# Kernel tuning notes

Hardware: AMD Instinct MI355X
Metric: run time of the kernel (lower is better)

## Reference

```python
import jax, jax.numpy as jnp
import numpy as np
from jax import lax

B, S, DM = 2, 2048, 2048
H, HKV, D = 16, 4, 128          # heads, kv heads, head_dim = DM // H
CLAMP_MAX = 0.95


def setup_inputs() -> dict:
    key = jax.random.key(0)
    k0, k1, k2, k3 = jax.random.split(key, 4)
    w_scale = 2 ** (-2.5) * (6.0 / (DM + DM)) ** 0.5  # xavier_uniform gain 2^-2.5 scale
    return {
        "hidden_states": jax.random.normal(k0, (B, S, DM), dtype=jnp.float32),
        "Wq": jax.random.uniform(k1, (DM, DM), jnp.float32, -w_scale, w_scale),
        "bq": jnp.zeros((DM,), jnp.float32),
        "Wk": jax.random.uniform(k2, (HKV * D, DM), jnp.float32, -w_scale, w_scale),
        "bk": jnp.zeros((HKV * D,), jnp.float32),
        "Wv": jax.random.uniform(k3, (HKV * D, DM), jnp.float32, -w_scale, w_scale),
        "bv": jnp.zeros((HKV * D,), jnp.float32),
    }


def _gla_forward(hidden_states, Wq, bq, Wk, bk, Wv, bv):
    b, s, _ = hidden_states.shape
    q = hidden_states @ Wq.T + bq                      # [b, s, H*D]
    k = hidden_states @ Wk.T + bk                      # [b, s, HKV*D]
    v = hidden_states @ Wv.T + bv                      # [b, s, HKV*D]
    q = q.reshape(b, s, H, D).transpose(0, 2, 1, 3)    # [b, H, s, D]
    k = k.reshape(b, s, HKV, D).transpose(0, 2, 1, 3)  # [b, HKV, s, D]
    v = v.reshape(b, s, HKV, D).transpose(0, 2, 1, 3)
    rep = H // HKV                                     # repeat_kv (GQA)
    k = jnp.repeat(k, rep, axis=1)                     # [b, H, s, D]
    v = jnp.repeat(v, rep, axis=1)
    q = jax.nn.relu(q)                                 # q_feature_map
    # layer_idx == 0 gate path: k = clamp(sigmoid(k), max=0.95); g = log(1 - k)
    kf = jnp.minimum(jax.nn.sigmoid(k.astype(jnp.float32)), CLAMP_MAX)
    g = jnp.log1p(-kf)                                 # log-space decay, g <= log(0.05) < 0 ... 0
    k = kf.astype(v.dtype)
    scale = D ** -0.5                                  # fla gla default scale = head_dim**-0.5
    q = (q * scale).astype(v.dtype)

    # GLA recurrence over time: S_t = exp(g_t)[:,None] * S_{t-1} + k_t^T v_t ; o_t = q_t S_t
    qs = q.transpose(2, 0, 1, 3)   # [s, b, H, D]
    ks = k.transpose(2, 0, 1, 3)
    vs = v.transpose(2, 0, 1, 3)
    gs = g.transpose(2, 0, 1, 3)

    def step(state, inp):           # state: [b, H, D, D] (key_dim x value_dim)
        qt, kt, vt, gt = inp
        state = state * jnp.exp(gt)[..., :, None] + kt[..., :, None] * vt[..., None, :]
        ot = jnp.einsum('bhd,bhde->bhe', qt, state)
        return state, ot

    S0 = jnp.zeros((b, H, D, D), jnp.float32)
    _, o = lax.scan(step, S0, (qs, ks, vs, gs))        # o: [s, b, H, D]
    o = o.transpose(1, 0, 2, 3).reshape(b, s, H * D)   # 'b h l d -> b l (h d)'
    return o


def reference(hidden_states, Wq, bq, Wk, bk, Wv, bv):
    return _gla_forward(hidden_states, Wq, bq, Wk, bk, Wv, bv)
```

## Files before the change

kernel.cpp:

```cpp
#include <hip/hip_runtime.h>
#include <math.h>

#define B_ 2
#define S_ 2048
#define DM_ 2048
#define H_ 16
#define HKV_ 4
#define D_ 128
#define NKV_ 512
#define M_ 4096
#define CHK_ 32
#define NC_ 64
#define SCALE_ 0.08838834764831845f
#define CLAMP_ 0.95f

typedef unsigned short u16;
typedef u16 ushortx8 __attribute__((ext_vector_type(8)));
typedef __bf16 bf16x8 __attribute__((ext_vector_type(8)));
typedef float f32x4 __attribute__((ext_vector_type(4)));

#define ASYNC16(gsrc, ldst) \
  __builtin_amdgcn_global_load_lds((const __attribute__((address_space(1))) void*)(gsrc), \
                                   (__attribute__((address_space(3))) void*)(ldst), 16, 0, 0)

__device__ __forceinline__ u16 f2b(float x){
  unsigned u = __float_as_uint(x);
  return (u16)((u + 0x7FFFu + ((u >> 16) & 1u)) >> 16);
}
__device__ __forceinline__ float b2f(u16 h){
  return __uint_as_float(((unsigned)h) << 16);
}
__device__ __forceinline__ bf16x8 ld8(const u16* p){
  return __builtin_bit_cast(bf16x8, *(const ushortx8*)p);
}
__device__ __forceinline__ f32x4 mfma16(bf16x8 a, bf16x8 b, f32x4 c){
  return __builtin_amdgcn_mfma_f32_16x16x32_bf16(a, b, c, 0, 0, 0);
}

__global__ void k_cvt_all(const float* __restrict__ hs, const float* __restrict__ Wq,
                          const float* __restrict__ Wk, const float* __restrict__ Wv,
                          u16* __restrict__ hsb, u16* __restrict__ wcb){
  int i = blockIdx.x * blockDim.x + threadIdx.x;
  const float* src; u16* dst;
  if (i < 1048576)      { src = hs + (size_t)i * 8;               dst = hsb + (size_t)i * 8; }
  else if (i < 1572864) { int j = i - 1048576; src = Wq + (size_t)j * 8; dst = wcb + (size_t)j * 8; }
  else if (i < 1703936) { int j = i - 1572864; src = Wk + (size_t)j * 8; dst = wcb + 4194304 + (size_t)j * 8; }
  else                  { int j = i - 1703936; src = Wv + (size_t)j * 8; dst = wcb + 5242880 + (size_t)j * 8; }
  const float4* p = (const float4*)src;
  float4 a = p[0], c = p[1];
  ushortx8 o;
  o[0]=f2b(a.x); o[1]=f2b(a.y); o[2]=f2b(a.z); o[3]=f2b(a.w);
  o[4]=f2b(c.x); o[5]=f2b(c.y); o[6]=f2b(c.z); o[7]=f2b(c.w);
  *(ushortx8*)dst = o;
}

__launch_bounds__(256, 2)
__global__ void k_gemm(const u16* __restrict__ A, const u16* __restrict__ W,
                       const float* __restrict__ bq, const float* __restrict__ bk,
                       const float* __restrict__ bv,
                       u16* __restrict__ qp, u16* __restrict__ kp,
                       float* __restrict__ gG, u16* __restrict__ vT){
  __shared__ u16 Al[128 * 32];
  __shared__ u16 Bl[128 * 32];
  const int tid = threadIdx.x;
  const int wid = tid >> 6, lane = tid & 63;
  const int m0 = blockIdx.y * 128, n0 = blockIdx.x * 128;
  const int wr = (wid >> 1) * 64, wc = (wid & 1) * 64;
  const int lr = lane & 15, lk = (lane >> 4) * 8;
  f32x4 acc[4][4] = {};
  for (int kt = 0; kt < 64; ++kt){
    const int k0 = kt * 32;
    #pragma unroll
    for (int s = 0; s < 2; ++s){
      const int fo = (wid * 2 + s) * 512;
      const int el = fo + lane * 8;
      const int row = el >> 5, kk = el & 31;
      ASYNC16(A + (size_t)(m0 + row) * DM_ + k0 + kk, Al + fo);
      ASYNC16(W + (size_t)(n0 + row) * DM_ + k0 + kk, Bl + fo);
    }
    __syncthreads();
    bf16x8 af[4], bfr[4];
    #pragma unroll
    for (int i = 0; i < 4; ++i) af[i]  = ld8(&Al[(wr + i*16 + lr)*32 + lk]);
    #pragma unroll
    for (int j = 0; j < 4; ++j) bfr[j] = ld8(&Bl[(wc + j*16 + lr)*32 + lk]);
    #pragma unroll
    for (int i = 0; i < 4; ++i)
      #pragma unroll
      for (int j = 0; j < 4; ++j)
        acc[i][j] = mfma16(af[i], bfr[j], acc[i][j]);
    __syncthreads();
  }
  const int lg4 = lane >> 4;
  const int tn = blockIdx.x;
  if (tn < 16){
    #pragma unroll
    for (int i = 0; i < 4; ++i){
      const int rb = m0 + wr + i*16 + lg4*4;
      #pragma unroll
      for (int j = 0; j < 4; ++j){
        const int col = n0 + wc + j*16 + lr;
        const float bb = bq[col];
        #pragma unroll
        for (int r = 0; r < 4; ++r){
          float q = fmaxf(acc[i][j][r] + bb, 0.f) * SCALE_;
          qp[(size_t)(rb + r) * DM_ + col] = f2b(q);
        }
      }
    }
  } else if (tn < 20){
    #pragma unroll
    for (int i = 0; i < 4; ++i){
      const int rb = m0 + wr + i*16 + lg4*4;
      #pragma unroll
      for (int j = 0; j < 4; ++j){
        const int cc = n0 - DM_ + wc + j*16 + lr;
        const float bb = bk[cc];
        #pragma unroll
        for (int r = 0; r < 4; ++r){
          float x = acc[i][j][r] + bb;
          float kf = fminf(1.f / (1.f + __expf(-x)), CLAMP_);
          kp[(size_t)(rb + r) * NKV_ + cc] = f2b(kf);
          gG[(size_t)(rb + r) * NKV_ + cc] = log1pf(-kf);
        }
      }
    }
  } else {
    #pragma unroll
    for (int i = 0; i < 4; ++i){
      const int rb = m0 + wr + i*16 + lg4*4;
      const int bb_ = rb >> 11;
      const int srow = rb & 2047;
      #pragma unroll
      for (int j = 0; j < 4; ++j){
        const int cc = n0 - DM_ - NKV_ + wc + j*16 + lr;
        const float bias = bv[cc];
        const int kv = cc >> 7, e = cc & 127;
        ushort4 pk;
        pk.x = f2b(acc[i][j][0] + bias);
        pk.y = f2b(acc[i][j][1] + bias);
        pk.z = f2b(acc[i][j][2] + bias);
        pk.w = f2b(acc[i][j][3] + bias);
        *(ushort4*)(vT + (((size_t)(bb_ * HKV_ + kv) * D_ + e) * S_ + srow)) = pk;
      }
    }
  }
}

__global__ void k_cumsum(float* __restrict__ g, float* __restrict__ dec){
  const int c = blockIdx.x, b = blockIdx.y;
  const int col = threadIdx.x;
  const size_t base = ((size_t)b * S_ + (size_t)c * CHK_) * NKV_ + col;
  float v[CHK_];
  #pragma unroll
  for (int t = 0; t < CHK_; ++t) v[t] = g[base + (size_t)t * NKV_];
  float acc = 0.f;
  #pragma unroll
  for (int t = 0; t < CHK_; ++t){ acc += v[t]; v[t] = acc; }
  #pragma unroll
  for (int t = 0; t < CHK_; ++t) g[base + (size_t)t * NKV_] = v[t];
  const int kv = col >> 7, d = col & 127;
  dec[(((size_t)b * HKV_ + kv) * NC_ + c) * D_ + d] = __expf(acc);
}

__launch_bounds__(256, 2)
__global__ void k_dstate(const u16* __restrict__ kp, const float* __restrict__ G,
                         const u16* __restrict__ vT, u16* __restrict__ SSt){
  __shared__ float kex[CHK_][D_];
  __shared__ float vl[D_][CHK_ + 1];
  const int c = blockIdx.x, kv = blockIdx.y, b = blockIdx.z;
  const int tid = threadIdx.x;
  const int s0 = c * CHK_;
  const size_t gbase = ((size_t)b * S_ + s0) * NKV_ + kv * D_;
  for (int idx = tid; idx < CHK_ * D_; idx += 256){
    const int t = idx >> 7, d = idx & 127;
    const float Gt  = G[gbase + (size_t)t  * NKV_ + d];
    const float G31 = G[gbase + (size_t)31 * NKV_ + d];
    const float kf = b2f(kp[gbase + (size_t)t * NKV_ + d]);
    kex[t][d] = kf * __expf(G31 - Gt);
  }
  const size_t vbase = ((size_t)(b * HKV_ + kv) * D_) * S_ + s0;
  for (int idx = tid; idx < 512; idx += 256){
    const int e = idx >> 2, t8 = (idx & 3) * 8;
    ushortx8 vv = *(const ushortx8*)(vT + vbase + (size_t)e * S_ + t8);
    #pragma unroll
    for (int u = 0; u < 8; ++u) vl[e][t8 + u] = b2f(vv[u]);
  }
  __syncthreads();
  const int w = tid >> 6, lane = tid & 63;
  const int e = (w & 1) * 64 + lane;
  const int d0 = (w >> 1) * 64;
  float acc[64];
  #pragma unroll
  for (int i = 0; i < 64; ++i) acc[i] = 0.f;
  for (int t = 0; t < CHK_; ++t){
    const float vv = vl[e][t];
    const float4* kr = (const float4*)(&kex[t][d0]);
    #pragma unroll
    for (int i4 = 0; i4 < 16; ++i4){
      float4 kk = kr[i4];
      acc[i4*4+0] = fmaf(vv, kk.x, acc[i4*4+0]);
      acc[i4*4+1] = fmaf(vv, kk.y, acc[i4*4+1]);
      acc[i4*4+2] = fmaf(vv, kk.z, acc[i4*4+2]);
      acc[i4*4+3] = fmaf(vv, kk.w, acc[i4*4+3]);
    }
  }
  const size_t ob = (((size_t)(b * HKV_ + kv) * NC_ + c) * D_ + e) * D_ + d0;
  #pragma unroll
  for (int i8 = 0; i8 < 8; ++i8){
    ushortx8 o;
    #pragma unroll
    for (int u = 0; u < 8; ++u) o[u] = f2b(acc[i8*8 + u]);
    *(ushortx8*)(SSt + ob + i8*8) = o;
  }
}

__global__ void k_scan(u16* __restrict__ SSt, const float* __restrict__ dec){
  const int eg = blockIdx.x, kv = blockIdx.y, b = blockIdx.z;
  const int tid = threadIdx.x;
  const int e = eg * 8 + (tid >> 5);
  const int d4 = (tid & 31) * 4;
  const size_t base  = ((size_t)(b * HKV_ + kv) * NC_) * D_ * D_ + (size_t)e * D_ + d4;
  const size_t dbase = ((size_t)(b * HKV_ + kv) * NC_) * D_ + d4;
  float s0 = 0.f, s1 = 0.f, s2 = 0.f, s3 = 0.f;
  #pragma unroll 4
  for (int c = 0; c < NC_; ++c){
    const size_t off = base + (size_t)c * (D_ * D_);
    ushort4 dv = *(ushort4*)(SSt + off);
    float4 dc = *(const float4*)(dec + dbase + (size_t)c * D_);
    ushort4 wr;
    wr.x = f2b(s0); wr.y = f2b(s1); wr.z = f2b(s2); wr.w = f2b(s3);
    *(ushort4*)(SSt + off) = wr;
    s0 = s0 * dc.x + b2f(dv.x);
    s1 = s1 * dc.y + b2f(dv.y);
    s2 = s2 * dc.z + b2f(dv.z);
    s3 = s3 * dc.w + b2f(dv.w);
  }
}

#define L_SB   0
#define L_KE0  16384
#define L_KE1  18432
#define L_QEF  22528
#define L_QE1  38912
#define L_AM   47104
#define L_G15  51200
__global__ void __launch_bounds__(512)
k_out2(const u16* __restrict__ qp, const u16* __restrict__ kp,
       const float* __restrict__ G, const u16* __restrict__ vT,
       const u16* __restrict__ SSt, float* __restrict__ out){
  extern __shared__ u16 lds[];
  float* G15f = (float*)(lds + L_G15);
  const int c = blockIdx.x, kv = blockIdx.y, b = blockIdx.z;
  const int tid = threadIdx.x, wid = tid >> 6, lane = tid & 63;
  const int hh = wid >> 1, sub = wid & 1;
  const int s0 = c * CHK_;
  const int lr = lane & 15, lk = (lane >> 4) * 8;
  const size_t gb = ((size_t)b * S_ + s0) * NKV_ + kv * D_;
  const size_t qb0 = ((size_t)b * S_ + s0) * DM_ + (kv * 4) * D_;
  const size_t vb = ((size_t)(b * HKV_ + kv) * D_) * S_ + s0;

  {
    const u16* src = SSt + (((size_t)(b * HKV_ + kv) * NC_ + c) * (D_ * D_));
    #pragma unroll
    for (int is = 0; is < 4; ++is){
      const int fo = is * 4096 + wid * 512;
      ASYNC16(src + fo + lane * 8, lds + L_SB + fo);
    }
  }
  if (tid < 128) G15f[tid] = G[gb + (size_t)15 * NKV_ + tid];
  __syncthreads();

  for (int idx = tid; idx < 32 * 128; idx += 512){
    const int t = idx >> 7, d = idx & 127;
    const float Gt = G[gb + (size_t)t * NKV_ + d];
    const float kf = b2f(kp[gb + (size_t)t * NKV_ + d]);
    const float eGt = __expf(Gt);
    float qv[4];
    #pragma unroll
    for (int q4 = 0; q4 < 4; ++q4) qv[q4] = b2f(qp[qb0 + (size_t)t * DM_ + q4 * D_ + d]);
    #pragma unroll
    for (int q4 = 0; q4 < 4; ++q4) lds[L_QEF + q4 * 4096 + idx] = f2b(qv[q4] * eGt);
    if (t >= 16){
      const float r = __expf(Gt - G15f[d]);
      #pragma unroll
      for (int q4 = 0; q4 < 4; ++q4) lds[L_QE1 + q4 * 2048 + (t - 16) * 128 + d] = f2b(qv[q4] * r);
    }
    if (t < 16) lds[L_KE0 + idx] = f2b(kf * __expf(-Gt));
    lds[L_KE1 + idx] = f2b(kf * __expf(G15f[d] - Gt));
  }
  __syncthreads();

  const u16* QeF = lds + L_QEF + hh * 4096;
  const u16* Qe1 = lds + L_QE1 + hh * 2048;
  u16* Am = lds + L_AM + hh * 1024;
  if (sub == 0){
    f32x4 aU = {}, aL = {};
    #pragma unroll
    for (int kd = 0; kd < 4; ++kd){
      bf16x8 faU = ld8(&QeF[lr * 128 + kd * 32 + lk]);
      bf16x8 fbU = ld8(&lds[L_KE0 + lr * 128 + kd * 32 + lk]);
      aU = mfma16(faU, fbU, aU);
      bf16x8 faL = ld8(&Qe1[lr * 128 + kd * 32 + lk]);
      bf16x8 fbL = ld8(&lds[L_KE1 + (16 + lr) * 128 + kd * 32 + lk]);
      aL = mfma16(faL, fbL, aL);
    }
    #pragma unroll
    for (int r = 0; r < 4; ++r){
      const int rr = (lane >> 4) * 4 + r;
      float vU = aU[r]; if (lr > rr) vU = 0.f;
      Am[rr * 32 + lr] = f2b(vU);
      float vL = aL[r]; if (lr > rr) vL = 0.f;
      Am[(16 + rr) * 32 + 16 + lr] = f2b(vL);
    }
  } else {
    f32x4 aO = {};
    #pragma unroll
    for (int kd = 0; kd < 4; ++kd){
      bf16x8 fa = ld8(&Qe1[lr * 128 + kd * 32 + lk]);
      bf16x8 fb = ld8(&lds[L_KE1 + lr * 128 + kd * 32 + lk]);
      aO = mfma16(fa, fb, aO);
    }
    #pragma unroll
    for (int r = 0; r < 4; ++r){
      const int rr = (lane >> 4) * 4 + r;
      Am[(16 + rr) * 32 + lr] = f2b(aO[r]);
    }
    for (int i = lane; i < 256; i += 64) Am[(i >> 4) * 32 + 16 + (i & 15)] = 0;
  }
  __syncthreads();

  f32x4 o4[2][4] = {};
  const int ew = sub * 64;
  #pragma unroll
  for (int kd = 0; kd < 4; ++kd){
    bf16x8 fa0 = ld8(&QeF[(0  + lr) * 128 + kd * 32 + lk]);
    bf16x8 fa1 = ld8(&QeF[(16 + lr) * 128 + kd * 32 + lk]);
    #pragma unroll
    for (int j2 = 0; j2 < 4; ++j2){
      bf16x8 fb = ld8(&lds[L_SB + (ew + j2 * 16 + lr) * 128 + kd * 32 + lk]);
      o4[0][j2] = mfma16(fa0, fb, o4[0][j2]);
      o4[1][j2] = mfma16(fa1, fb, o4[1][j2]);
    }
  }
  {
    bf16x8 fa0 = ld8(&Am[lr * 32 + lk]);
    bf16x8 fa1 = ld8(&Am[(16 + lr) * 32 + lk]);
    #pragma unroll
    for (int j2 = 0; j2 < 4; ++j2){
      const u16* vr = vT + vb + (size_t)(ew + j2 * 16 + lr) * S_;
      bf16x8 fb = ld8(vr + lk);
      o4[0][j2] = mfma16(fa0, fb, o4[0][j2]);
      o4[1][j2] = mfma16(fa1, fb, o4[1][j2]);
    }
  }
  const int hD = (kv * 4 + hh) * D_;
  #pragma unroll
  for (int i2 = 0; i2 < 2; ++i2)
    #pragma unroll
    for (int j2 = 0; j2 < 4; ++j2)
      #pragma unroll
      for (int r = 0; r < 4; ++r){
        const int t = i2 * 16 + (lane >> 4) * 4 + r;
        const int e = ew + j2 * 16 + lr;
        out[((size_t)b * S_ + s0 + t) * DM_ + hD + e] = o4[i2][j2][r];
      }
}

extern "C" void kernel_launch(void* const* d_in, const int* in_sizes, int n_in,
                              void* d_out, int out_size, void* d_ws, size_t ws_size,
                              hipStream_t stream){
  const float* hs = (const float*)d_in[0];
  const float* Wq = (const float*)d_in[1];
  const float* bq = (const float*)d_in[2];
  const float* Wk = (const float*)d_in[3];
  const float* bk = (const float*)d_in[4];
  const float* Wv = (const float*)d_in[5];
  const float* bv = (const float*)d_in[6];
  char* ws = (char*)d_ws;
  u16*   hsb = (u16*)(ws);
  u16*   wcb = (u16*)(ws + 16777216);
  u16*   qp  = (u16*)(ws + 29360128);
  u16*   kp  = (u16*)(ws + 46137344);
  float* gG  = (float*)(ws + 50331648);
  u16*   vT  = (u16*)(ws + 58720256);
  float* dec = (float*)(ws + 62914560);
  u16*   SSt = (u16*)(ws + 63176704);
  float* out = (float*)d_out;

  hipFuncSetAttribute((const void*)k_out2,
                      hipFuncAttributeMaxDynamicSharedMemorySize, 102912);

  k_cvt_all<<<dim3(7168), 256, 0, stream>>>(hs, Wq, Wk, Wv, hsb, wcb);
  k_gemm<<<dim3(24, 32), 256, 0, stream>>>(hsb, wcb, bq, bk, bv, qp, kp, gG, vT);
  k_cumsum<<<dim3(NC_, B_), 512, 0, stream>>>(gG, dec);
  k_dstate<<<dim3(NC_, HKV_, B_), 256, 0, stream>>>(kp, gG, vT, SSt);
  k_scan<<<dim3(16, HKV_, B_), 256, 0, stream>>>(SSt, dec);
  k_out2<<<dim3(NC_, HKV_, B_), 512, 102912, stream>>>(qp, kp, gG, vT, SSt, out);
}
```

Before: 152.1 us.

## Triple-buffer GEMM LDS tiles with async prefetch two stages ahead

Replaces the single-buffered LDS staging in the projection GEMM with a three-slot ring. Tiles are prefetched two K-steps ahead via global_load_lds, and a manual vmcnt wait plus one barrier per iteration replaces the two __syncthreads. The aim is to overlap global loads with MFMA work instead of stalling on each tile. It raises LDS use to 48KB per block, which may limit occupancy under launch_bounds(256,2). It also relies on exact vmcnt accounting and issues redundant clamped loads for the last tiles.

```diff
diff --git a/kernel.cpp b/kernel.cpp
--- a/kernel.cpp
+++ b/kernel.cpp
@@ -22,6 +22,8 @@
 #define ASYNC16(gsrc, ldst) \
   __builtin_amdgcn_global_load_lds((const __attribute__((address_space(1))) void*)(gsrc), \
                                    (__attribute__((address_space(3))) void*)(ldst), 16, 0, 0)
+#define SBAR()    __builtin_amdgcn_s_barrier()
+#define WAITV(n)  asm volatile("s_waitcnt vmcnt(" #n ")" ::: "memory")
 
 __device__ __forceinline__ u16 f2b(float x){
   unsigned u = __float_as_uint(x);
@@ -60,37 +62,57 @@
                        const float* __restrict__ bv,
                        u16* __restrict__ qp, u16* __restrict__ kp,
                        float* __restrict__ gG, u16* __restrict__ vT){
-  __shared__ u16 Al[128 * 32];
-  __shared__ u16 Bl[128 * 32];
+  __shared__ u16 L[3 * 8192];
   const int tid = threadIdx.x;
   const int wid = tid >> 6, lane = tid & 63;
   const int m0 = blockIdx.y * 128, n0 = blockIdx.x * 128;
   const int wr = (wid >> 1) * 64, wc = (wid & 1) * 64;
   const int lr = lane & 15, lk = (lane >> 4) * 8;
+
+  int offA[4], offB[4];
+  #pragma unroll
+  for (int m = 0; m < 4; ++m) offA[m] = (wr + m * 16 + lr) * 32 + lk;
+  #pragma unroll
+  for (int n = 0; n < 4; ++n) offB[n] = (wc + n * 16 + lr) * 32 + lk;
+
+  const int srow = wid * 32 + (lane >> 2);
+  const int scol = (lane & 3) * 8;
+  const u16* gA = A + (size_t)(m0 + srow) * DM_ + scol;
+  const u16* gW = W + (size_t)(n0 + srow) * DM_ + scol;
+  const int fo = wid * 1024;
+
+#define STG(db, kk0) \
+  ASYNC16(gA + (kk0),             L + (db) + fo); \
+  ASYNC16(gA + 16 * DM_ + (kk0),  L + (db) + fo + 512); \
+  ASYNC16(gW + (kk0),             L + (db) + 4096 + fo); \
+  ASYNC16(gW + 16 * DM_ + (kk0),  L + (db) + 4096 + fo + 512)
+
   f32x4 acc[4][4] = {};
+
+  STG(0, 0);
+  STG(8192, 32);
+
+  int sl_cur = 0, sl_st = 16384;
   for (int kt = 0; kt < 64; ++kt){
-    const int k0 = kt * 32;
-    #pragma unroll
-    for (int s = 0; s < 2; ++s){
-      const int fo = (wid * 2 + s) * 512;
-      const int el = fo + lane * 8;
-      const int row = el >> 5, kk = el & 31;
-      ASYNC16(A + (size_t)(m0 + row) * DM_ + k0 + kk, Al + fo);
-      ASYNC16(W + (size_t)(n0 + row) * DM_ + k0 + kk, Bl + fo);
-    }
-    __syncthreads();
-    bf16x8 af[4], bfr[4];
-    #pragma unroll
-    for (int i = 0; i < 4; ++i) af[i]  = ld8(&Al[(wr + i*16 + lr)*32 + lk]);
-    #pragma unroll
-    for (int j = 0; j < 4; ++j) bfr[j] = ld8(&Bl[(wc + j*16 + lr)*32 + lk]);
-    #pragma unroll
-    for (int i = 0; i < 4; ++i)
-      #pragma unroll
-      for (int j = 0; j < 4; ++j)
-        acc[i][j] = mfma16(af[i], bfr[j], acc[i][j]);
-    __syncthreads();
-  }
+    WAITV(4);
+    SBAR();
+    const int k2 = ((kt + 2 < 64) ? kt + 2 : 63) * 32;
+    STG(sl_st, k2);
+    bf16x8 af[4], bfv[4];
+    #pragma unroll
+    for (int m = 0; m < 4; ++m) af[m]  = ld8(L + sl_cur + offA[m]);
+    #pragma unroll
+    for (int n = 0; n < 4; ++n) bfv[n] = ld8(L + sl_cur + 4096 + offB[n]);
+    #pragma unroll
+    for (int m = 0; m < 4; ++m)
+      #pragma unroll
+      for (int n = 0; n < 4; ++n)
+        acc[m][n] = mfma16(af[m], bfv[n], acc[m][n]);
+    sl_cur = (sl_cur == 16384) ? 0 : sl_cur + 8192;
+    sl_st  = (sl_st  == 16384) ? 0 : sl_st  + 8192;
+  }
+#undef STG
+
   const int lg4 = lane >> 4;
   const int tn = blockIdx.x;
   if (tn < 16){
@@ -130,7 +152,7 @@
     for (int i = 0; i < 4; ++i){
       const int rb = m0 + wr + i*16 + lg4*4;
       const int bb_ = rb >> 11;
-      const int srow = rb & 2047;
+      const int srw = rb & 2047;
       #pragma unroll
       for (int j = 0; j < 4; ++j){
         const int cc = n0 - DM_ - NKV_ + wc + j*16 + lr;
@@ -141,7 +163,7 @@
         pk.y = f2b(acc[i][j][1] + bias);
         pk.z = f2b(acc[i][j][2] + bias);
         pk.w = f2b(acc[i][j][3] + bias);
-        *(ushort4*)(vT + (((size_t)(bb_ * HKV_ + kv) * D_ + e) * S_ + srow)) = pk;
+        *(ushort4*)(vT + (((size_t)(bb_ * HKV_ + kv) * D_ + e) * S_ + srw)) = pk;
       }
     }
   }
```

New measurement: 151.9 us. No clear change (-0.2%).
